# Optimization experiments

Hardware: AMD Instinct MI355X
Metric: run time of the kernel (lower is better)

## Reference

```python
import jax, jax.numpy as jnp
import numpy as np

N_NODES = 100000
N_EDGES = 1600000
D_FEAT = 128
HIDDEN = 64


def setup_inputs() -> dict:
    key = jax.random.key(0)
    k1, k2, k3, k4, k5 = jax.random.split(key, 5)
    x = jax.random.normal(k1, (N_NODES, D_FEAT), dtype=jnp.float32)
    edge_index = jax.random.randint(k2, (2, N_EDGES), 0, N_NODES, dtype=jnp.int32)
    edge_weight = jax.random.uniform(k3, (N_EDGES,), dtype=jnp.float32)
    W1 = jax.random.normal(k4, (D_FEAT, HIDDEN), dtype=jnp.float32) / np.sqrt(D_FEAT)
    b1 = jnp.zeros((HIDDEN,), dtype=jnp.float32)
    W2 = jax.random.normal(k5, (HIDDEN, 1), dtype=jnp.float32) / np.sqrt(HIDDEN)
    b2 = jnp.zeros((1,), dtype=jnp.float32)
    return {"x": x, "edge_index": edge_index, "edge_weight": edge_weight,
            "W1": W1, "b1": b1, "W2": W2, "b2": b2}


def reference(x, edge_index, edge_weight, W1, b1, W2, b2):
    N = x.shape[0]
    # PyG GCNConv default: add self-loops with weight 1.0
    loops = jnp.arange(N, dtype=edge_index.dtype)
    row = jnp.concatenate([edge_index[0], loops])  # source nodes
    col = jnp.concatenate([edge_index[1], loops])  # target nodes
    ew = jnp.concatenate([edge_weight, jnp.ones((N,), dtype=edge_weight.dtype)])
    # symmetric degree normalization: norm_e = d^{-1/2}[row] * w_e * d^{-1/2}[col]
    deg = jax.ops.segment_sum(ew, col, num_segments=N)
    dinv = jnp.where(deg > 0, jax.lax.rsqrt(deg), 0.0)
    norm = dinv[row] * ew * dinv[col]  # [E+N]

    def gcn_layer(h, W, b):
        h = h @ W                          # [N, out] transform first (PyG order)
        msg = h[row] * norm[:, None]       # gather + scale, [E+N, out]
        agg = jax.ops.segment_sum(msg, col, num_segments=N)  # scatter-add
        return agg + b

    h = jax.nn.relu(gcn_layer(x, W1, b1))
    # dropout(p=0.5) is identity in eval mode
    return gcn_layer(h, W2, b2)  # [N, 1]
```

## Files before the change

### kernel.cpp

```cpp
#include <hip/hip_runtime.h>
#include <stdint.h>

typedef float f4 __attribute__((ext_vector_type(4)));
typedef float f32x4 __attribute__((ext_vector_type(4)));
typedef _Float16 hq4 __attribute__((ext_vector_type(4)));
typedef _Float16 half8 __attribute__((ext_vector_type(8)));

#define DF 128
#define HID 64
#define EPB 4096
#define CAP 5120

__global__ __launch_bounds__(256) void kPrep(const float* __restrict__ W1,
                                             _Float16* __restrict__ W1f,
                                             int* __restrict__ cur, int nbin) {
    int t = blockIdx.x * 256 + threadIdx.x;
    if (t < nbin) cur[t] = 0;
    if (t < 8192) {
        int j     = t & 7;
        int lane  = (t >> 3) & 63;
        int ntile = (t >> 9) & 3;
        int kstep = t >> 11;
        int k = kstep * 32 + (lane >> 4) * 8 + j;
        int n = ntile * 16 + (lane & 15);
        W1f[t] = (_Float16)W1[k * 64 + n];
    }
}

__global__ __launch_bounds__(512) void kA3(const int* __restrict__ row,
                                           const int* __restrict__ col,
                                           const float* __restrict__ ew,
                                           int* __restrict__ cur,
                                           int2* __restrict__ tmp,
                                           int E, int nbin) {
    __shared__ int hist[512];
    __shared__ int pref[512];
    __shared__ int lbase[512];
    __shared__ int2 sv[EPB];
    __shared__ int  sa[EPB];
    int b = blockIdx.x, t = threadIdx.x;
    hist[t] = 0;
    __syncthreads();
    int s = b * EPB, e = min(E, s + EPB);
    int cnt = e - s;
    int  mybin[8], myrank[8];
    int2 myv[8];
#pragma unroll
    for (int k = 0; k < 8; ++k) {
        int i = s + t + k * 512;
        mybin[k] = -1;
        if (i < e) {
            int c = col[i];
            int bin = c >> 8;
            myv[k].x = row[i] | ((c & 255) << 24);
            myv[k].y = __float_as_int(ew[i]);
            mybin[k] = bin;
            myrank[k] = atomicAdd(&hist[bin], 1);
        }
    }
    __syncthreads();
    int val = hist[t];
    lbase[t] = val ? atomicAdd(&cur[t], val) + t * CAP : 0;
    for (int d = 1; d < 512; d <<= 1) {
        int x = (t >= d) ? hist[t - d] : 0;
        __syncthreads();
        hist[t] += x;
        __syncthreads();
    }
    pref[t] = hist[t] - val;
    __syncthreads();
#pragma unroll
    for (int k = 0; k < 8; ++k) {
        if (mybin[k] >= 0) {
            int pos = pref[mybin[k]] + myrank[k];
            sv[pos] = myv[k];
            sa[pos] = lbase[mybin[k]] + myrank[k];
        }
    }
    __syncthreads();
    for (int i = t; i < cnt; i += 512) tmp[sa[i]] = sv[i];
}

__global__ __launch_bounds__(256) void kB(const int2* __restrict__ tmp,
                                          const int* __restrict__ cur,
                                          int2* __restrict__ edata,
                                          int2* __restrict__ offse,
                                          float* __restrict__ dinv,
                                          int N) {
    __shared__ int hist[256];
    __shared__ int basel[256];
    __shared__ int startl[256];
    __shared__ float degl[256];
    __shared__ int2 sorted[CAP];
    int bin = blockIdx.x, t = threadIdx.x;
    int s = bin * CAP;
    int cnt = min(cur[bin], CAP);
    int e = s + cnt;

    hist[t] = 0;
    degl[t] = 0.f;
    __syncthreads();
    for (int i = s + t; i < e; i += 256) {
        int2 pr = tmp[i];
        int lo = ((unsigned)pr.x) >> 24;
        atomicAdd(&hist[lo], 1);
        atomicAdd(&degl[lo], __int_as_float(pr.y));
    }
    __syncthreads();
    int val = hist[t];
    __syncthreads();
    for (int d = 1; d < 256; d <<= 1) {
        int x = (t >= d) ? hist[t - d] : 0;
        __syncthreads();
        hist[t] += x;
        __syncthreads();
    }
    int loff = hist[t] - val;
    startl[t] = s + loff;
    basel[t]  = loff;
    __syncthreads();
    for (int i = s + t; i < e; i += 256) {
        int2 pr = tmp[i];
        int lo = ((unsigned)pr.x) >> 24;
        int pos = atomicAdd(&basel[lo], 1);
        int2 o;
        o.x = pr.x & 0x00FFFFFF;
        o.y = pr.y;
        sorted[pos] = o;
    }
    __syncthreads();
    for (int i = t; i < cnt; i += 256) edata[s + i] = sorted[i];
    int c = bin * 256 + t;
    if (c < N) {
        int2 oe;
        oe.x = startl[t];
        oe.y = startl[t] + val;
        offse[c] = oe;
        dinv[c] = rsqrtf(1.0f + degl[t]);
    }
}

__global__ __launch_bounds__(256) void k_gemm1(const float* __restrict__ x,
                                               const _Float16* __restrict__ W1f,
                                               const float* __restrict__ dinv,
                                               _Float16* __restrict__ h, int N) {
    int wave  = (blockIdx.x * 256 + threadIdx.x) >> 6;
    int nstrip = (N + 15) >> 4;
    if (wave >= nstrip) return;
    int node0 = wave << 4;
    int l = threadIdx.x & 63;
    int quad = l >> 4;
    int m = l & 15;
    int r = node0 + m;
    if (r >= N) r = N - 1;

    const half8* bfrag = (const half8*)W1f;
    f32x4 acc[4];
#pragma unroll
    for (int nt = 0; nt < 4; ++nt) acc[nt] = (f32x4)(0.f);

#pragma unroll
    for (int kstep = 0; kstep < 4; ++kstep) {
        const f4* xr = (const f4*)(x + (size_t)r * DF + kstep * 32 + quad * 8);
        f4 a0 = xr[0], a1 = xr[1];
        half8 af;
        af[0] = (_Float16)a0.x; af[1] = (_Float16)a0.y;
        af[2] = (_Float16)a0.z; af[3] = (_Float16)a0.w;
        af[4] = (_Float16)a1.x; af[5] = (_Float16)a1.y;
        af[6] = (_Float16)a1.z; af[7] = (_Float16)a1.w;
#pragma unroll
        for (int nt = 0; nt < 4; ++nt) {
            half8 bf = bfrag[(kstep * 4 + nt) * 64 + l];
            acc[nt] = __builtin_amdgcn_mfma_f32_16x16x32_f16(af, bf, acc[nt], 0, 0, 0);
        }
    }

    float dv[4];
    int nodeb = node0 + quad * 4;
#pragma unroll
    for (int reg = 0; reg < 4; ++reg)
        dv[reg] = (nodeb + reg < N) ? dinv[nodeb + reg] : 0.f;
#pragma unroll
    for (int nt = 0; nt < 4; ++nt) {
#pragma unroll
        for (int reg = 0; reg < 4; ++reg) {
            int node = nodeb + reg;
            if (node < N)
                h[(unsigned)node * 64u + (unsigned)(nt * 16 + m)] =
                    (_Float16)(dv[reg] * acc[nt][reg]);
        }
    }
}

__global__ __launch_bounds__(256) void k_agg_h2(const int2* __restrict__ offse,
                                                const int2* __restrict__ edata,
                                                const float* __restrict__ dinv,
                                                const _Float16* __restrict__ h,
                                                const float* __restrict__ b1,
                                                const float* __restrict__ W2,
                                                float* __restrict__ h2p, int N) {
    __shared__ int2 stage[4][64];
    int wv = threadIdx.x >> 6;
    int v = blockIdx.x * 4 + wv;
    if (v >= N) return;
    int l = threadIdx.x & 63;
    int sub = l >> 4;
    unsigned fq = (unsigned)(l & 15);
    const hq4* hp = (const hq4*)h;

    float di = dinv[v];
    float a0 = 0.f, a1 = 0.f, a2 = 0.f, a3 = 0.f;
    if (sub == 0) {
        hq4 sv4 = hp[((unsigned)v << 4) | fq];
        a0 = (float)sv4.x; a1 = (float)sv4.y;
        a2 = (float)sv4.z; a3 = (float)sv4.w;
    }

    int2 oe = offse[v];
    for (int base = oe.x; base < oe.y; base += 64) {
        int idx = base + l;
        int2 pr;
        pr.x = 0; pr.y = 0;
        if (idx < oe.y) pr = edata[idx];
        stage[wv][l] = pr;
        int cnt = min(64, oe.y - base);
        int steps = (cnt + 3) >> 2;
#pragma unroll 4
        for (int k = 0; k < steps; ++k) {
            int2 em = stage[wv][4 * k + sub];
            float w = __int_as_float(em.y);
            hq4 hv = hp[((unsigned)em.x << 4) | fq];
            a0 += w * (float)hv.x;
            a1 += w * (float)hv.y;
            a2 += w * (float)hv.z;
            a3 += w * (float)hv.w;
        }
    }
    a0 += __shfl_xor(a0, 16); a1 += __shfl_xor(a1, 16);
    a2 += __shfl_xor(a2, 16); a3 += __shfl_xor(a3, 16);
    a0 += __shfl_xor(a0, 32); a1 += __shfl_xor(a1, 32);
    a2 += __shfl_xor(a2, 32); a3 += __shfl_xor(a3, 32);

    if (sub == 0) {
        a0 = di * a0; a1 = di * a1; a2 = di * a2; a3 = di * a3;
        float s = fmaxf(a0 + b1[4 * fq], 0.f)     * W2[4 * fq]
                + fmaxf(a1 + b1[4 * fq + 1], 0.f) * W2[4 * fq + 1]
                + fmaxf(a2 + b1[4 * fq + 2], 0.f) * W2[4 * fq + 2]
                + fmaxf(a3 + b1[4 * fq + 3], 0.f) * W2[4 * fq + 3];
        s += __shfl_down(s, 8);
        s += __shfl_down(s, 4);
        s += __shfl_down(s, 2);
        s += __shfl_down(s, 1);
        if (fq == 0) h2p[v] = di * s;
    }
}

__global__ __launch_bounds__(256) void k_out(const int2* __restrict__ offse,
                                             const int2* __restrict__ edata,
                                             const float* __restrict__ dinv,
                                             const float* __restrict__ h2p,
                                             const float* __restrict__ b2,
                                             float* __restrict__ out, int N) {
    int t = blockIdx.x * 256 + threadIdx.x;
    int v = t >> 4;
    if (v >= N) return;
    int c = t & 15;
    int2 oe = offse[v];
    float s = 0.f;
    for (int i = oe.x + c; i < oe.y; i += 16) {
        int2 pr = edata[i];
        s += __int_as_float(pr.y) * h2p[(unsigned)pr.x];
    }
    s += __shfl_down(s, 8);
    s += __shfl_down(s, 4);
    s += __shfl_down(s, 2);
    s += __shfl_down(s, 1);
    if (c == 0) {
        float di = dinv[v];
        out[v] = b2[0] + di * (h2p[v] + s);
    }
}

extern "C" void kernel_launch(void* const* d_in, const int* in_sizes, int n_in,
                              void* d_out, int out_size, void* d_ws, size_t ws_size,
                              hipStream_t stream) {
    const float* x  = (const float*)d_in[0];
    const int*   ei = (const int*)d_in[1];
    const float* ew = (const float*)d_in[2];
    const float* W1 = (const float*)d_in[3];
    const float* b1 = (const float*)d_in[4];
    const float* W2 = (const float*)d_in[5];
    const float* b2 = (const float*)d_in[6];
    float* out = (float*)d_out;

    const int N = in_sizes[0] / DF;
    const int E = in_sizes[2];
    const int* row = ei;
    const int* col = ei + E;

    const int nbin = (N + 255) / 256;
    const int nblk = (E + EPB - 1) / EPB;

    size_t    gsz   = (size_t)nbin * CAP;
    int*      w32   = (int*)d_ws;
    int2*     edata = (int2*)w32;
    int*      shreg = w32 + (size_t)2 * gsz;
    int2*     tmp   = (int2*)shreg;
    _Float16* h     = (_Float16*)shreg;
    int*      p     = shreg + (size_t)2 * gsz;
    int*      cur   = p;  p += ((nbin) + 3) & ~3;
    float*    dinv  = (float*)p;  p += N;
    float*    h2p   = (float*)p;  p += N;
    int2*     offse = (int2*)p;   p += 2 * N;
    _Float16* W1f   = (_Float16*)p;

    const int B = 256;
    int nstrip = (N + 15) / 16;
    int gGm  = (nstrip + 3) / 4;
    int gAgg = (N + 3) / 4;
    int gN16 = (N * 16 + B - 1) / B;

    kPrep<<<32, B, 0, stream>>>(W1, W1f, cur, nbin);
    kA3<<<nblk, 512, 0, stream>>>(row, col, ew, cur, tmp, E, nbin);
    kB<<<nbin, B, 0, stream>>>(tmp, cur, edata, offse, dinv, N);
    k_gemm1<<<gGm, B, 0, stream>>>(x, W1f, dinv, h, N);
    k_agg_h2<<<gAgg, B, 0, stream>>>(offse, edata, dinv, h, b1, W2, h2p, N);
    k_out<<<gN16, B, 0, stream>>>(offse, edata, dinv, h2p, b2, out, N);
}
```

Measured before the change: 207.2 us.

## Stage bin edges in LDS, widen kB, and aggregate output per bin

kB now runs 512 threads per bin and copies each bin's edges into LDS once, so the second pass no longer rereads global memory. It also keeps the local target id in the high byte of edata, so the aggregation kernel must mask the source index. k_out changes from 16 threads per node reading offsets to one block per bin that streams the bin's edges linearly and accumulates with LDS atomics. This makes the final pass a coalesced sweep, at the cost of LDS atomic contention and more LDS per block in kB, which can reduce occupancy.

```diff
diff --git a/kernel.cpp b/kernel.cpp
--- a/kernel.cpp
+++ b/kernel.cpp
@@ -10,6 +10,7 @@
 #define HID 64
 #define EPB 4096
 #define CAP 5120
+#define SRCMASK 0x00FFFFFF
 
 __global__ __launch_bounds__(256) void kPrep(const float* __restrict__ W1,
                                              _Float16* __restrict__ W1f,
@@ -81,60 +82,55 @@
     for (int i = t; i < cnt; i += 512) tmp[sa[i]] = sv[i];
 }
 
-__global__ __launch_bounds__(256) void kB(const int2* __restrict__ tmp,
+__global__ __launch_bounds__(512) void kB(const int2* __restrict__ tmp,
                                           const int* __restrict__ cur,
                                           int2* __restrict__ edata,
                                           int2* __restrict__ offse,
                                           float* __restrict__ dinv,
                                           int N) {
+    __shared__ int2 raw[CAP];
+    __shared__ int2 sorted[CAP];
     __shared__ int hist[256];
     __shared__ int basel[256];
-    __shared__ int startl[256];
     __shared__ float degl[256];
-    __shared__ int2 sorted[CAP];
     int bin = blockIdx.x, t = threadIdx.x;
     int s = bin * CAP;
     int cnt = min(cur[bin], CAP);
-    int e = s + cnt;
-
-    hist[t] = 0;
-    degl[t] = 0.f;
-    __syncthreads();
-    for (int i = s + t; i < e; i += 256) {
-        int2 pr = tmp[i];
+
+    if (t < 256) { hist[t] = 0; degl[t] = 0.f; }
+    __syncthreads();
+    for (int i = t; i < cnt; i += 512) {
+        int2 pr = tmp[s + i];
+        raw[i] = pr;
         int lo = ((unsigned)pr.x) >> 24;
         atomicAdd(&hist[lo], 1);
         atomicAdd(&degl[lo], __int_as_float(pr.y));
     }
     __syncthreads();
-    int val = hist[t];
+    int val = (t < 256) ? hist[t] : 0;
     __syncthreads();
     for (int d = 1; d < 256; d <<= 1) {
-        int x = (t >= d) ? hist[t - d] : 0;
+        int x = (t < 256 && t >= d) ? hist[t - d] : 0;
         __syncthreads();
-        hist[t] += x;
+        if (t < 256) hist[t] += x;
         __syncthreads();
     }
-    int loff = hist[t] - val;
-    startl[t] = s + loff;
-    basel[t]  = loff;
-    __syncthreads();
-    for (int i = s + t; i < e; i += 256) {
-        int2 pr = tmp[i];
+    if (t < 256) basel[t] = hist[t] - val;
+    __syncthreads();
+    for (int i = t; i < cnt; i += 512) {
+        int2 pr = raw[i];
         int lo = ((unsigned)pr.x) >> 24;
         int pos = atomicAdd(&basel[lo], 1);
-        int2 o;
-        o.x = pr.x & 0x00FFFFFF;
-        o.y = pr.y;
-        sorted[pos] = o;
-    }
-    __syncthreads();
-    for (int i = t; i < cnt; i += 256) edata[s + i] = sorted[i];
+        sorted[pos] = pr;
+    }
+    __syncthreads();
+    for (int i = t; i < cnt; i += 512) edata[s + i] = sorted[i];
     int c = bin * 256 + t;
-    if (c < N) {
+    if (t < 256 && c < N) {
+        int end = basel[t];
         int2 oe;
-        oe.x = startl[t];
-        oe.y = startl[t] + val;
+        oe.x = s + end - val;
+        oe.y = s + end;
         offse[c] = oe;
         dinv[c] = rsqrtf(1.0f + degl[t]);
     }
@@ -229,7 +225,8 @@
         for (int k = 0; k < steps; ++k) {
             int2 em = stage[wv][4 * k + sub];
             float w = __int_as_float(em.y);
-            hq4 hv = hp[((unsigned)em.x << 4) | fq];
+            unsigned src = (unsigned)(em.x & SRCMASK);
+            hq4 hv = hp[(src << 4) | fq];
             a0 += w * (float)hv.x;
             a1 += w * (float)hv.y;
             a2 += w * (float)hv.z;
@@ -255,30 +252,27 @@
     }
 }
 
-__global__ __launch_bounds__(256) void k_out(const int2* __restrict__ offse,
+__global__ __launch_bounds__(256) void k_out(const int* __restrict__ cur,
                                              const int2* __restrict__ edata,
                                              const float* __restrict__ dinv,
                                              const float* __restrict__ h2p,
                                              const float* __restrict__ b2,
                                              float* __restrict__ out, int N) {
-    int t = blockIdx.x * 256 + threadIdx.x;
-    int v = t >> 4;
-    if (v >= N) return;
-    int c = t & 15;
-    int2 oe = offse[v];
-    float s = 0.f;
-    for (int i = oe.x + c; i < oe.y; i += 16) {
+    __shared__ float acc[256];
+    int bin = blockIdx.x, t = threadIdx.x;
+    acc[t] = 0.f;
+    __syncthreads();
+    int s = bin * CAP;
+    int cnt = min(cur[bin], CAP);
+    for (int i = s + t; i < s + cnt; i += 256) {
         int2 pr = edata[i];
-        s += __int_as_float(pr.y) * h2p[(unsigned)pr.x];
-    }
-    s += __shfl_down(s, 8);
-    s += __shfl_down(s, 4);
-    s += __shfl_down(s, 2);
-    s += __shfl_down(s, 1);
-    if (c == 0) {
-        float di = dinv[v];
-        out[v] = b2[0] + di * (h2p[v] + s);
-    }
+        int lo = ((unsigned)pr.x) >> 24;
+        float val = __int_as_float(pr.y) * h2p[(unsigned)(pr.x & SRCMASK)];
+        atomicAdd(&acc[lo], val);
+    }
+    __syncthreads();
+    int v = bin * 256 + t;
+    if (v < N) out[v] = b2[0] + dinv[v] * (h2p[v] + acc[t]);
 }
 
 extern "C" void kernel_launch(void* const* d_in, const int* in_sizes, int n_in,
@@ -318,12 +312,11 @@
     int nstrip = (N + 15) / 16;
     int gGm  = (nstrip + 3) / 4;
     int gAgg = (N + 3) / 4;
-    int gN16 = (N * 16 + B - 1) / B;
 
     kPrep<<<32, B, 0, stream>>>(W1, W1f, cur, nbin);
     kA3<<<nblk, 512, 0, stream>>>(row, col, ew, cur, tmp, E, nbin);
-    kB<<<nbin, B, 0, stream>>>(tmp, cur, edata, offse, dinv, N);
+    kB<<<nbin, 512, 0, stream>>>(tmp, cur, edata, offse, dinv, N);
     k_gemm1<<<gGm, B, 0, stream>>>(x, W1f, dinv, h, N);
     k_agg_h2<<<gAgg, B, 0, stream>>>(offse, edata, dinv, h, b1, W2, h2p, N);
-    k_out<<<gN16, B, 0, stream>>>(offse, edata, dinv, h2p, b2, out, N);
-}
+    k_out<<<nbin, B, 0, stream>>>(cur, edata, dinv, h2p, b2, out, N);
+}
```

New measurement: 212.1 us. 1.02x slower.
